# Performance work log

Measured on AMD Instinct MI355X. Metric: run time of the kernel, lower is better.

The kernel has to match this reference:

```python
import jax, jax.numpy as jnp
import numpy as np

B, P, D, K, NCLS = 32, 1024, 3, 5, 2  # graphs, points/graph, input dim, knn, classes
EPS = 1e-5


def _bn(x, g, be):
    # BatchNorm1d in training mode: stats over all axes except channel (torch flattens edges/nodes to rows)
    ax = tuple(range(x.ndim - 1))
    m = jnp.mean(x, axis=ax, keepdims=True)
    v = jnp.mean((x - m) ** 2, axis=ax, keepdims=True)
    return g * (x - m) / jnp.sqrt(v + EPS) + be


def _mlp(x, layers):
    for w, b, g, be in layers:  # Seq(Lin, ReLU, BN)
        x = _bn(jax.nn.relu(x @ w + b), g, be)
    return x


def _knn(x, k):
    # x: [B,P,d] -> idx [B,P,k] of k nearest neighbours (self included, as torch_cluster.knn)
    sq = jnp.sum(x * x, axis=-1)
    d2 = sq[:, :, None] + sq[:, None, :] - 2.0 * jnp.einsum('bpd,bqd->bpq', x, x)
    _, idx = jax.lax.top_k(-d2, k)
    return idx


def _edge_conv(x, k, layers):
    # DynamicEdgeConv: knn graph on current features, msg = nn([x_i, x_j - x_i]), max-aggregate
    idx = _knn(x, k)                                      # [B,P,k]
    xj = jax.vmap(lambda xb, ib: xb[ib])(x, idx)          # [B,P,k,d]
    xi = jnp.broadcast_to(x[:, :, None, :], xj.shape)
    e = jnp.concatenate([xi, xj - xi], axis=-1)           # [B,P,k,2d]
    e = _mlp(e, layers)
    return jnp.max(e, axis=2)                             # max aggr over neighbours


def setup_inputs() -> dict:
    key = jax.random.key(0)
    ks = iter(jax.random.split(key, 40))
    def w(shape):
        return jax.random.normal(next(ks), shape, jnp.float32) * 0.1
    inp = {}
    inp['pos'] = jax.random.normal(next(ks), (B * P, D), jnp.float32)
    inp['batch'] = jnp.repeat(jnp.arange(B, dtype=jnp.int32), P)
    for i, (a, c) in enumerate([(2 * D, 64), (64, 64), (64, 64)], 1):
        inp[f'c1_w{i}'] = w((a, c)); inp[f'c1_b{i}'] = w((c,))
        inp[f'c1_g{i}'] = jnp.ones((c,), jnp.float32); inp[f'c1_be{i}'] = jnp.zeros((c,), jnp.float32)
    inp['c2_w1'] = w((128, 128)); inp['c2_b1'] = w((128,))
    inp['c2_g1'] = jnp.ones((128,), jnp.float32); inp['c2_be1'] = jnp.zeros((128,), jnp.float32)
    inp['l1_w'] = w((192, 1024)); inp['l1_b'] = w((1024,))
    inp['l1_g'] = jnp.ones((1024,), jnp.float32); inp['l1_be'] = jnp.zeros((1024,), jnp.float32)
    inp['m1_w'] = w((1024, 512)); inp['m1_b'] = w((512,))
    inp['m1_g'] = jnp.ones((512,), jnp.float32); inp['m1_be'] = jnp.zeros((512,), jnp.float32)
    inp['m2_w'] = w((512, 256)); inp['m2_b'] = w((256,))
    inp['m2_g'] = jnp.ones((256,), jnp.float32); inp['m2_be'] = jnp.zeros((256,), jnp.float32)
    inp['m3_w'] = w((256, NCLS)); inp['m3_b'] = w((NCLS,))
    return inp


def reference(pos, batch, c1_w1, c1_b1, c1_g1, c1_be1, c1_w2, c1_b2, c1_g2, c1_be2, c1_w3, c1_b3, c1_g3, c1_be3, c2_w1, c2_b1, c2_g1, c2_be1, l1_w, l1_b, l1_g, l1_be, m1_w, m1_b, m1_g, m1_be, m2_w, m2_b, m2_g, m2_be, m3_w, m3_b):
    # equal-sized graphs: batch vector is jnp.repeat(arange(B), P), so reshape is exact
    x = pos.reshape(B, P, D)
    x1 = _edge_conv(x, K, [(c1_w1, c1_b1, c1_g1, c1_be1), (c1_w2, c1_b2, c1_g2, c1_be2), (c1_w3, c1_b3, c1_g3, c1_be3)])  # [B,P,64]
    x2 = _edge_conv(x1, K, [(c2_w1, c2_b1, c2_g1, c2_be1)])  # [B,P,128]
    out = _mlp(jnp.concatenate([x1, x2], axis=-1), [(l1_w, l1_b, l1_g, l1_be)])  # [B,P,1024]
    out = jnp.max(out, axis=1)  # global_max_pool -> [B,1024]
    out = _mlp(out, [(m1_w, m1_b, m1_g, m1_be), (m2_w, m2_b, m2_g, m2_be)])
    return out @ m3_w + m3_b  # [B, n_classes]
```

## Files before the change

kernel.cpp:

```cpp
#include <hip/hip_runtime.h>


#define NB 32
#define NP 1024
#define NPT 32768
#define KNN 5
#define NE 163840

#define FINF 3.402823466e+38f

typedef __attribute__((ext_vector_type(8))) short bf16x8;
typedef __attribute__((ext_vector_type(4))) float f32x4;

__device__ __forceinline__ bool lex_less(float da, int ja, float db, int jb) {
  return (da < db) || (da == db && ja < jb);
}

__device__ __forceinline__ float f4c(const float4& v, int q) {
  return q == 0 ? v.x : (q == 1 ? v.y : (q == 2 ? v.z : v.w));
}

__device__ __forceinline__ ushort f2bf(float f) {
  union { float f; unsigned u; } v; v.f = f;
  unsigned r = (v.u + 0x7FFFu + ((v.u >> 16) & 1u)) >> 16;
  return (ushort)r;
}
__device__ __forceinline__ float bf2f(ushort h) {
  union { unsigned u; float f; } v; v.u = ((unsigned)h) << 16;
  return v.f;
}

__device__ __forceinline__ void insert5(float& d0, float& d1, float& d2, float& d3, float& d4,
                                        int& j0, int& j1, int& j2, int& j3, int& j4,
                                        float dd, int jj) {
  if (lex_less(dd, jj, d4, j4)) {
    bool L0 = lex_less(dd,jj,d0,j0), L1 = lex_less(dd,jj,d1,j1),
         L2 = lex_less(dd,jj,d2,j2), L3 = lex_less(dd,jj,d3,j3);
    d4 = L3 ? d3 : dd;              j4 = L3 ? j3 : jj;
    d3 = L3 ? (L2 ? d2 : dd) : d3;  j3 = L3 ? (L2 ? j2 : jj) : j3;
    d2 = L2 ? (L1 ? d1 : dd) : d2;  j2 = L2 ? (L1 ? j1 : jj) : j2;
    d1 = L1 ? (L0 ? d0 : dd) : d1;  j1 = L1 ? (L0 ? j0 : jj) : j1;
    d0 = L0 ? dd : d0;              j0 = L0 ? jj : j0;
  }
}

__device__ __forceinline__ void insert5f(float& d0, float& d1, float& d2, float& d3, float& d4,
                                         int& j0, int& j1, int& j2, int& j3, int& j4,
                                         float dd, int jj) {
  if (dd < d4) {
    bool L0 = dd < d0, L1 = dd < d1, L2 = dd < d2, L3 = dd < d3;
    d4 = L3 ? d3 : dd;              j4 = L3 ? j3 : jj;
    d3 = L3 ? (L2 ? d2 : dd) : d3;  j3 = L3 ? (L2 ? j2 : jj) : j3;
    d2 = L2 ? (L1 ? d1 : dd) : d2;  j2 = L2 ? (L1 ? j1 : jj) : j2;
    d1 = L1 ? (L0 ? d0 : dd) : d1;  j1 = L1 ? (L0 ? j0 : jj) : j1;
    d0 = L0 ? dd : d0;              j0 = L0 ? jj : j0;
  }
}

__global__ __launch_bounds__(256) void knn1_kernel(const float* __restrict__ pos,
                                                   int* __restrict__ knn_idx) {
  __shared__ float4 xs4[NP];
  const int b = blockIdx.x >> 5;
  const int seg = blockIdx.x & 31;
  const int t = threadIdx.x;
  for (int i = t; i < NP; i += 256) {
    float x0 = pos[(size_t)b*NP*3 + i*3 + 0];
    float x1 = pos[(size_t)b*NP*3 + i*3 + 1];
    float x2 = pos[(size_t)b*NP*3 + i*3 + 2];
    float sq = __fadd_rn(__fadd_rn(__fmul_rn(x0,x0), __fmul_rn(x1,x1)), __fmul_rn(x2,x2));
    xs4[i] = make_float4(x0, x1, x2, sq);
  }
  __syncthreads();
  const int q = t >> 3;
  const int ql = t & 7;
  const int i = seg * 32 + q;
  const float4 xi = xs4[i];
  const float sqi = xi.w;
  float d0=FINF,d1=FINF,d2=FINF,d3=FINF,d4=FINF;
  int j0=0x7fffffff,j1=0x7fffffff,j2=0x7fffffff,j3=0x7fffffff,j4=0x7fffffff;
  for (int jj = 0; jj < NP/8; ++jj) {
    const int j = jj*8 + ql;
    float4 v = xs4[j];
    float dot = __fadd_rn(__fadd_rn(__fmul_rn(xi.x,v.x), __fmul_rn(xi.y,v.y)), __fmul_rn(xi.z,v.z));
    float dd = __fsub_rn(__fadd_rn(sqi, v.w), __fmul_rn(2.0f, dot));
    insert5f(d0,d1,d2,d3,d4, j0,j1,j2,j3,j4, dd, j);
  }
  #pragma unroll
  for (int m = 1; m <= 4; m <<= 1) {
    float e0 = __shfl_xor(d0, m, 8), e1 = __shfl_xor(d1, m, 8),
          e2 = __shfl_xor(d2, m, 8), e3 = __shfl_xor(d3, m, 8),
          e4 = __shfl_xor(d4, m, 8);
    int   k0 = __shfl_xor(j0, m, 8), k1 = __shfl_xor(j1, m, 8),
          k2 = __shfl_xor(j2, m, 8), k3 = __shfl_xor(j3, m, 8),
          k4 = __shfl_xor(j4, m, 8);
    insert5(d0,d1,d2,d3,d4, j0,j1,j2,j3,j4, e0, k0);
    insert5(d0,d1,d2,d3,d4, j0,j1,j2,j3,j4, e1, k1);
    insert5(d0,d1,d2,d3,d4, j0,j1,j2,j3,j4, e2, k2);
    insert5(d0,d1,d2,d3,d4, j0,j1,j2,j3,j4, e3, k3);
    insert5(d0,d1,d2,d3,d4, j0,j1,j2,j3,j4, e4, k4);
  }
  if (ql == 0) {
    const size_t row = (size_t)b * NP + i;
    knn_idx[row*KNN+0] = b*NP + j0;
    knn_idx[row*KNN+1] = b*NP + j1;
    knn_idx[row*KNN+2] = b*NP + j2;
    knn_idx[row*KNN+3] = b*NP + j3;
    knn_idx[row*KNN+4] = b*NP + j4;
  }
}

__global__ __launch_bounds__(256) void ec1_l1_kernel(const float* __restrict__ pos,
    const int* __restrict__ knn_idx, const float* __restrict__ W,
    const float* __restrict__ bias, float* __restrict__ hout,
    double* __restrict__ psum, double* __restrict__ psq) {
  __shared__ float ef[64][6];
  __shared__ float Wl[6][64];
  __shared__ float bl[64];
  __shared__ double red[256];
  const int blk = blockIdx.x, t = threadIdx.x;
  const int ebase = blk * 64;
  if (t < 64) {
    int e = ebase + t;
    int ip = e / KNN;
    int jp = knn_idx[e];
    float a0 = pos[(size_t)ip*3+0], a1 = pos[(size_t)ip*3+1], a2 = pos[(size_t)ip*3+2];
    float c0 = pos[(size_t)jp*3+0], c1 = pos[(size_t)jp*3+1], c2 = pos[(size_t)jp*3+2];
    ef[t][0] = a0; ef[t][1] = a1; ef[t][2] = a2;
    ef[t][3] = c0 - a0; ef[t][4] = c1 - a1; ef[t][5] = c2 - a2;
    bl[t] = bias[t];
  }
  for (int idx = t; idx < 6*64; idx += 256) Wl[idx>>6][idx&63] = W[idx];
  __syncthreads();
  const int c = t & 63, rs = t >> 6;
  double s = 0.0, ss = 0.0;
  for (int r = rs; r < 64; r += 4) {
    float acc = bl[c];
    #pragma unroll
    for (int q = 0; q < 6; ++q) acc = fmaf(ef[r][q], Wl[q][c], acc);
    acc = fmaxf(acc, 0.0f);
    hout[(size_t)(ebase + r)*64 + c] = acc;
    s += acc; ss += (double)acc * (double)acc;
  }
  red[t] = s; __syncthreads();
  if (t < 64) psum[(size_t)blk*64 + t] = red[t] + red[t+64] + red[t+128] + red[t+192];
  __syncthreads();
  red[t] = ss; __syncthreads();
  if (t < 64) psq[(size_t)blk*64 + t] = red[t] + red[t+64] + red[t+128] + red[t+192];
}

__global__ __launch_bounds__(256) void stats_reduce_kernel(const double* __restrict__ psum,
    const double* __restrict__ psq, int nblk, int C, double invN,
    const float* __restrict__ g, const float* __restrict__ be,
    float2* __restrict__ aff) {
  __shared__ double rs[256];
  __shared__ double rq[256];
  const int c = blockIdx.x;
  const int t = threadIdx.x;
  double s = 0.0, ss = 0.0;
  for (int i = t; i < nblk; i += 256) {
    s  += psum[(size_t)i*C + c];
    ss += psq [(size_t)i*C + c];
  }
  rs[t] = s; rq[t] = ss; __syncthreads();
  for (int off = 128; off > 0; off >>= 1) {
    if (t < off) { rs[t] += rs[t+off]; rq[t] += rq[t+off]; }
    __syncthreads();
  }
  if (t == 0) {
    double mean = rs[0] * invN;
    double var = rq[0] * invN - mean*mean;
    var = var < 0.0 ? 0.0 : var;
    double inv = 1.0 / sqrt(var + 1e-5);
    float a = (float)((double)g[c] * inv);
    float off2 = (float)((double)be[c] - (double)g[c] * mean * inv);
    aff[c] = make_float2(a, off2);
  }
}

__global__ __launch_bounds__(256) void ec_l64_kernel(const float* __restrict__ hin,
    const float2* __restrict__ affprev, const float* __restrict__ W,
    const float* __restrict__ bias, float* __restrict__ hout,
    double* __restrict__ psum, double* __restrict__ psq) {
  __shared__ float ein[64][68];
  __shared__ float Wl[64][64];
  __shared__ float2 affl[64];
  __shared__ float bl[64];
  __shared__ double redS[16][64];
  __shared__ double redQ[16][64];
  const int blk = blockIdx.x, t = threadIdx.x;
  const size_t ebase = (size_t)blk * 64;
  if (t < 64) { affl[t] = affprev[t]; bl[t] = bias[t]; }
  __syncthreads();
  for (int idx = t; idx < 64*64; idx += 256) {
    int r = idx >> 6, c = idx & 63;
    float2 ac = affl[c];
    ein[r][c] = fmaf(hin[ebase*64 + idx], ac.x, ac.y);
    Wl[r][c] = W[idx];
  }
  __syncthreads();
  const int c4 = t & 15, rs = t >> 4;
  const int cbase = c4 * 4;
  const int rbase = rs * 4;
  float acc[4][4];
  #pragma unroll
  for (int ii = 0; ii < 4; ++ii) {
    #pragma unroll
    for (int jj = 0; jj < 4; ++jj) acc[ii][jj] = bl[cbase + jj];
  }
  for (int cin = 0; cin < 64; cin += 4) {
    float4 fi[4];
    #pragma unroll
    for (int ii = 0; ii < 4; ++ii) fi[ii] = *(const float4*)&ein[rbase+ii][cin];
    #pragma unroll
    for (int q = 0; q < 4; ++q) {
      float4 wv = *(const float4*)&Wl[cin+q][cbase];
      #pragma unroll
      for (int ii = 0; ii < 4; ++ii) {
        float f = f4c(fi[ii], q);
        acc[ii][0] = fmaf(f, wv.x, acc[ii][0]);
        acc[ii][1] = fmaf(f, wv.y, acc[ii][1]);
        acc[ii][2] = fmaf(f, wv.z, acc[ii][2]);
        acc[ii][3] = fmaf(f, wv.w, acc[ii][3]);
      }
    }
  }
  double s[4] = {0,0,0,0}, ss[4] = {0,0,0,0};
  #pragma unroll
  for (int ii = 0; ii < 4; ++ii) {
    float4 h;
    h.x = fmaxf(acc[ii][0], 0.f); h.y = fmaxf(acc[ii][1], 0.f);
    h.z = fmaxf(acc[ii][2], 0.f); h.w = fmaxf(acc[ii][3], 0.f);
    *(float4*)&hout[(ebase + rbase + ii)*64 + cbase] = h;
    s[0]+=h.x; s[1]+=h.y; s[2]+=h.z; s[3]+=h.w;
    ss[0]+=(double)h.x*h.x; ss[1]+=(double)h.y*h.y;
    ss[2]+=(double)h.z*h.z; ss[3]+=(double)h.w*h.w;
  }
  #pragma unroll
  for (int jj = 0; jj < 4; ++jj) { redS[rs][cbase+jj] = s[jj]; redQ[rs][cbase+jj] = ss[jj]; }
  __syncthreads();
  if (t < 64) {
    double a = 0, bq = 0;
    #pragma unroll
    for (int r = 0; r < 16; ++r) { a += redS[r][t]; bq += redQ[r][t]; }
    psum[(size_t)blk*64 + t] = a;
    psq[(size_t)blk*64 + t] = bq;
  }
}

__global__ __launch_bounds__(256) void ec_l64_last_kernel(const float* __restrict__ hin,
    const float2* __restrict__ affprev, const float* __restrict__ W,
    const float* __restrict__ bias, float* __restrict__ hmax, float* __restrict__ hmin,
    double* __restrict__ psum, double* __restrict__ psq) {
  __shared__ float ein[80][68];
  __shared__ float Wl[64][64];
  __shared__ float2 affl[64];
  __shared__ float bl[64];
  double (*redS)[64] = (double (*)[64])(&ein[0][0]);
  double (*redQ)[64] = (double (*)[64])((char*)&ein[0][0] + 8192);
  const int blk = blockIdx.x, t = threadIdx.x;
  const size_t ebase = (size_t)blk * 80;
  if (t < 64) { affl[t] = affprev[t]; bl[t] = bias[t]; }
  __syncthreads();
  for (int idx = t; idx < 80*64; idx += 256) {
    int r = idx >> 6, c = idx & 63;
    float2 ac = affl[c];
    ein[r][c] = fmaf(hin[ebase*64 + idx], ac.x, ac.y);
  }
  for (int idx = t; idx < 64*64; idx += 256) Wl[idx>>6][idx&63] = W[idx];
  __syncthreads();
  const int c4 = t & 15, rs = t >> 4;
  const int cbase = c4 * 4;
  const int rbase = rs * 5;
  float acc[5][4];
  #pragma unroll
  for (int ii = 0; ii < 5; ++ii) {
    #pragma unroll
    for (int jj = 0; jj < 4; ++jj) acc[ii][jj] = bl[cbase + jj];
  }
  for (int cin = 0; cin < 64; cin += 4) {
    float4 fi[5];
    #pragma unroll
    for (int ii = 0; ii < 5; ++ii) fi[ii] = *(const float4*)&ein[rbase+ii][cin];
    #pragma unroll
    for (int q = 0; q < 4; ++q) {
      float4 wv = *(const float4*)&Wl[cin+q][cbase];
      #pragma unroll
      for (int ii = 0; ii < 5; ++ii) {
        float f = f4c(fi[ii], q);
        acc[ii][0] = fmaf(f, wv.x, acc[ii][0]);
        acc[ii][1] = fmaf(f, wv.y, acc[ii][1]);
        acc[ii][2] = fmaf(f, wv.z, acc[ii][2]);
        acc[ii][3] = fmaf(f, wv.w, acc[ii][3]);
      }
    }
  }
  float4 mx = make_float4(-FINF,-FINF,-FINF,-FINF);
  float4 mn = make_float4(FINF,FINF,FINF,FINF);
  double s[4] = {0,0,0,0}, ss[4] = {0,0,0,0};
  #pragma unroll
  for (int ii = 0; ii < 5; ++ii) {
    float4 h;
    h.x = fmaxf(acc[ii][0], 0.f); h.y = fmaxf(acc[ii][1], 0.f);
    h.z = fmaxf(acc[ii][2], 0.f); h.w = fmaxf(acc[ii][3], 0.f);
    mx.x = fmaxf(mx.x, h.x); mn.x = fminf(mn.x, h.x);
    mx.y = fmaxf(mx.y, h.y); mn.y = fminf(mn.y, h.y);
    mx.z = fmaxf(mx.z, h.z); mn.z = fminf(mn.z, h.z);
    mx.w = fmaxf(mx.w, h.w); mn.w = fminf(mn.w, h.w);
    s[0]+=h.x; s[1]+=h.y; s[2]+=h.z; s[3]+=h.w;
    ss[0]+=(double)h.x*h.x; ss[1]+=(double)h.y*h.y;
    ss[2]+=(double)h.z*h.z; ss[3]+=(double)h.w*h.w;
  }
  *(float4*)&hmax[((size_t)blk*16 + rs)*64 + cbase] = mx;
  *(float4*)&hmin[((size_t)blk*16 + rs)*64 + cbase] = mn;
  __syncthreads();
  #pragma unroll
  for (int jj = 0; jj < 4; ++jj) { redS[rs][cbase+jj] = s[jj]; redQ[rs][cbase+jj] = ss[jj]; }
  __syncthreads();
  if (t < 64) {
    double a = 0, bq = 0;
    #pragma unroll
    for (int r = 0; r < 16; ++r) { a += redS[r][t]; bq += redQ[r][t]; }
    psum[(size_t)blk*64 + t] = a;
    psq[(size_t)blk*64 + t] = bq;
  }
}

__global__ __launch_bounds__(256) void x1c_kernel(const float* __restrict__ hmax,
    const float* __restrict__ hmin, const float2* __restrict__ aff,
    float* __restrict__ x1, ushort* __restrict__ x1hi, ushort* __restrict__ x1lo,
    float* __restrict__ sqg) {
  __shared__ float xs[16][65];
  const int blk = blockIdx.x, t = threadIdx.x;
  const size_t base = (size_t)blk * 16 * 64;
  const int o = t * 4;
  const int c4 = o & 63;
  float4 vmx = *(const float4*)&hmax[base + o];
  float4 vmn = *(const float4*)&hmin[base + o];
  float2 a0 = aff[c4+0], a1 = aff[c4+1], a2 = aff[c4+2], a3 = aff[c4+3];
  float4 xv;
  xv.x = (a0.x >= 0.f) ? fmaf(a0.x, vmx.x, a0.y) : fmaf(a0.x, vmn.x, a0.y);
  xv.y = (a1.x >= 0.f) ? fmaf(a1.x, vmx.y, a1.y) : fmaf(a1.x, vmn.y, a1.y);
  xv.z = (a2.x >= 0.f) ? fmaf(a2.x, vmx.z, a2.y) : fmaf(a2.x, vmn.z, a2.y);
  xv.w = (a3.x >= 0.f) ? fmaf(a3.x, vmx.w, a3.y) : fmaf(a3.x, vmn.w, a3.y);
  *(float4*)&x1[base + o] = xv;
  ushort4 h, lo;
  h.x = f2bf(xv.x); lo.x = f2bf(xv.x - bf2f(h.x));
  h.y = f2bf(xv.y); lo.y = f2bf(xv.y - bf2f(h.y));
  h.z = f2bf(xv.z); lo.z = f2bf(xv.z - bf2f(h.z));
  h.w = f2bf(xv.w); lo.w = f2bf(xv.w - bf2f(h.w));
  *(ushort4*)&x1hi[base + o] = h;
  *(ushort4*)&x1lo[base + o] = lo;
  const int r = o >> 6;
  xs[r][c4+0] = xv.x; xs[r][c4+1] = xv.y; xs[r][c4+2] = xv.z; xs[r][c4+3] = xv.w;
  __syncthreads();
  if (t < 16) {
    float s = 0.f;
    #pragma unroll
    for (int c = 0; c < 64; ++c) s = fmaf(xs[t][c], xs[t][c], s);
    sqg[(size_t)blk*16 + t] = s;
  }
}

__global__ __launch_bounds__(256) void knn2_kernel(const ushort* __restrict__ x1hi,
    const ushort* __restrict__ x1lo, const float* __restrict__ sqg,
    float* __restrict__ kpd, int* __restrict__ kpj) {
  __shared__ __align__(16) char smem[36864];
  ushort* xihi = (ushort*)smem;
  ushort* xilo = (ushort*)(smem + 9216);
  ushort* xjhi = (ushort*)(smem + 18432);
  ushort* xjlo = (ushort*)(smem + 27648);
  float*  dist = (float*)(smem + 18432);
  const int b = blockIdx.x >> 5;
  const int it = (blockIdx.x >> 1) & 15;
  const int half = blockIdx.x & 1;
  const int t = threadIdx.x;
  const int ibase = it * 64;

  #pragma unroll
  for (int i = 0; i < 2; ++i) {
    int idx = i*256 + t;
    int r = idx >> 3, c8 = (idx & 7) * 8;
    *(bf16x8*)&xihi[r*72 + c8] = *(const bf16x8*)&x1hi[((size_t)b*NP + ibase + r)*64 + c8];
    *(bf16x8*)&xilo[r*72 + c8] = *(const bf16x8*)&x1lo[((size_t)b*NP + ibase + r)*64 + c8];
  }

  const int w = t >> 6, l = t & 63;
  const int lr = l & 15, lg = l >> 4;
  const int row = t >> 2, ql = t & 3;
  float si2[4];
  #pragma unroll
  for (int ii = 0; ii < 4; ++ii)
    si2[ii] = sqg[(size_t)b*NP + ibase + w*16 + lg*4 + ii];

  float d0=FINF,d1=FINF,d2=FINF,d3=FINF,d4=FINF;
  int j0=0x7fffffff,j1=0x7fffffff,j2=0x7fffffff,j3=0x7fffffff,j4=0x7fffffff;

  for (int jt = 0; jt < 8; ++jt) {
    const int jtg = half * 8 + jt;
    __syncthreads();
    #pragma unroll
    for (int i = 0; i < 2; ++i) {
      int idx = i*256 + t;
      int r = idx >> 3, c8 = (idx & 7) * 8;
      *(bf16x8*)&xjhi[r*72 + c8] = *(const bf16x8*)&x1hi[((size_t)b*NP + jtg*64 + r)*64 + c8];
      *(bf16x8*)&xjlo[r*72 + c8] = *(const bf16x8*)&x1lo[((size_t)b*NP + jtg*64 + r)*64 + c8];
    }
    __syncthreads();
    f32x4 acc0 = (f32x4){0.f,0.f,0.f,0.f};
    f32x4 acc1 = (f32x4){0.f,0.f,0.f,0.f};
    f32x4 acc2 = (f32x4){0.f,0.f,0.f,0.f};
    f32x4 acc3 = (f32x4){0.f,0.f,0.f,0.f};
    #pragma unroll
    for (int ks = 0; ks < 2; ++ks) {
      const int k0 = ks * 32;
      bf16x8 ah = *(const bf16x8*)&xihi[(w*16 + lr)*72 + k0 + lg*8];
      bf16x8 al = *(const bf16x8*)&xilo[(w*16 + lr)*72 + k0 + lg*8];
      {
        bf16x8 bh = *(const bf16x8*)&xjhi[(0*16 + lr)*72 + k0 + lg*8];
        bf16x8 bl = *(const bf16x8*)&xjlo[(0*16 + lr)*72 + k0 + lg*8];
        acc0 = __builtin_amdgcn_mfma_f32_16x16x32_bf16(ah, bh, acc0, 0, 0, 0);
        acc0 = __builtin_amdgcn_mfma_f32_16x16x32_bf16(ah, bl, acc0, 0, 0, 0);
        acc0 = __builtin_amdgcn_mfma_f32_16x16x32_bf16(al, bh, acc0, 0, 0, 0);
        acc0 = __builtin_amdgcn_mfma_f32_16x16x32_bf16(al, bl, acc0, 0, 0, 0);
      }
      {
        bf16x8 bh = *(const bf16x8*)&xjhi[(1*16 + lr)*72 + k0 + lg*8];
        bf16x8 bl = *(const bf16x8*)&xjlo[(1*16 + lr)*72 + k0 + lg*8];
        acc1 = __builtin_amdgcn_mfma_f32_16x16x32_bf16(ah, bh, acc1, 0, 0, 0);
        acc1 = __builtin_amdgcn_mfma_f32_16x16x32_bf16(ah, bl, acc1, 0, 0, 0);
        acc1 = __builtin_amdgcn_mfma_f32_16x16x32_bf16(al, bh, acc1, 0, 0, 0);
        acc1 = __builtin_amdgcn_mfma_f32_16x16x32_bf16(al, bl, acc1, 0, 0, 0);
      }
      {
        bf16x8 bh = *(const bf16x8*)&xjhi[(2*16 + lr)*72 + k0 + lg*8];
        bf16x8 bl = *(const bf16x8*)&xjlo[(2*16 + lr)*72 + k0 + lg*8];
        acc2 = __builtin_amdgcn_mfma_f32_16x16x32_bf16(ah, bh, acc2, 0, 0, 0);
        acc2 = __builtin_amdgcn_mfma_f32_16x16x32_bf16(ah, bl, acc2, 0, 0, 0);
        acc2 = __builtin_amdgcn_mfma_f32_16x16x32_bf16(al, bh, acc2, 0, 0, 0);
        acc2 = __builtin_amdgcn_mfma_f32_16x16x32_bf16(al, bl, acc2, 0, 0, 0);
      }
      {
        bf16x8 bh = *(const bf16x8*)&xjhi[(3*16 + lr)*72 + k0 + lg*8];
        bf16x8 bl = *(const bf16x8*)&xjlo[(3*16 + lr)*72 + k0 + lg*8];
        acc3 = __builtin_amdgcn_mfma_f32_16x16x32_bf16(ah, bh, acc3, 0, 0, 0);
        acc3 = __builtin_amdgcn_mfma_f32_16x16x32_bf16(ah, bl, acc3, 0, 0, 0);
        acc3 = __builtin_amdgcn_mfma_f32_16x16x32_bf16(al, bh, acc3, 0, 0, 0);
        acc3 = __builtin_amdgcn_mfma_f32_16x16x32_bf16(al, bl, acc3, 0, 0, 0);
      }
    }
    float sjv0 = sqg[(size_t)b*NP + jtg*64 + 0*16 + lr];
    float sjv1 = sqg[(size_t)b*NP + jtg*64 + 1*16 + lr];
    float sjv2 = sqg[(size_t)b*NP + jtg*64 + 2*16 + lr];
    float sjv3 = sqg[(size_t)b*NP + jtg*64 + 3*16 + lr];
    __syncthreads();
    #pragma unroll
    for (int ii = 0; ii < 4; ++ii) {
      const int irow = w*16 + lg*4 + ii;
      dist[irow*68 + 0*16 + lr] = fmaf(-2.f, acc0[ii], si2[ii] + sjv0);
      dist[irow*68 + 1*16 + lr] = fmaf(-2.f, acc1[ii], si2[ii] + sjv1);
      dist[irow*68 + 2*16 + lr] = fmaf(-2.f, acc2[ii], si2[ii] + sjv2);
      dist[irow*68 + 3*16 + lr] = fmaf(-2.f, acc3[ii], si2[ii] + sjv3);
    }
    __syncthreads();
    const int jgbase = jtg*64 + ql*16;
    #pragma unroll
    for (int kk = 0; kk < 4; ++kk) {
      float4 v = *(const float4*)&dist[row*68 + ql*16 + 4*kk];
      insert5f(d0,d1,d2,d3,d4, j0,j1,j2,j3,j4, v.x, jgbase + 4*kk + 0);
      insert5f(d0,d1,d2,d3,d4, j0,j1,j2,j3,j4, v.y, jgbase + 4*kk + 1);
      insert5f(d0,d1,d2,d3,d4, j0,j1,j2,j3,j4, v.z, jgbase + 4*kk + 2);
      insert5f(d0,d1,d2,d3,d4, j0,j1,j2,j3,j4, v.w, jgbase + 4*kk + 3);
    }
  }

  #pragma unroll
  for (int m = 1; m <= 2; m <<= 1) {
    float e0 = __shfl_xor(d0, m, 4), e1 = __shfl_xor(d1, m, 4),
          e2 = __shfl_xor(d2, m, 4), e3 = __shfl_xor(d3, m, 4),
          e4 = __shfl_xor(d4, m, 4);
    int   k0 = __shfl_xor(j0, m, 4), k1 = __shfl_xor(j1, m, 4),
          k2 = __shfl_xor(j2, m, 4), k3 = __shfl_xor(j3, m, 4),
          k4 = __shfl_xor(j4, m, 4);
    insert5(d0,d1,d2,d3,d4, j0,j1,j2,j3,j4, e0, k0);
    insert5(d0,d1,d2,d3,d4, j0,j1,j2,j3,j4, e1, k1);
    insert5(d0,d1,d2,d3,d4, j0,j1,j2,j3,j4, e2, k2);
    insert5(d0,d1,d2,d3,d4, j0,j1,j2,j3,j4, e3, k3);
    insert5(d0,d1,d2,d3,d4, j0,j1,j2,j3,j4, e4, k4);
  }
  if (ql == 0) {
    const size_t orow = ((size_t)half*NPT + (size_t)b*NP + ibase + row) * KNN;
    kpd[orow+0] = d0; kpd[orow+1] = d1; kpd[orow+2] = d2; kpd[orow+3] = d3; kpd[orow+4] = d4;
    kpj[orow+0] = j0; kpj[orow+1] = j1; kpj[orow+2] = j2; kpj[orow+3] = j3; kpj[orow+4] = j4;
  }
}

__global__ void knn2_merge_kernel(const float* __restrict__ kpd,
    const int* __restrict__ kpj, int* __restrict__ knn_idx) {
  int r = blockIdx.x * 256 + threadIdx.x;
  if (r >= NPT) return;
  const int b = r >> 10;
  const size_t r0 = (size_t)r * KNN;
  const size_t r1 = ((size_t)NPT + r) * KNN;
  float d0 = kpd[r0+0], d1 = kpd[r0+1], d2 = kpd[r0+2], d3 = kpd[r0+3], d4 = kpd[r0+4];
  int   j0 = kpj[r0+0], j1 = kpj[r0+1], j2 = kpj[r0+2], j3 = kpj[r0+3], j4 = kpj[r0+4];
  #pragma unroll
  for (int s = 0; s < KNN; ++s) {
    insert5(d0,d1,d2,d3,d4, j0,j1,j2,j3,j4, kpd[r1+s], kpj[r1+s]);
  }
  knn_idx[r0+0] = b*NP + j0;
  knn_idx[r0+1] = b*NP + j1;
  knn_idx[r0+2] = b*NP + j2;
  knn_idx[r0+3] = b*NP + j3;
  knn_idx[r0+4] = b*NP + j4;
}

__global__ __launch_bounds__(256) void wt2_kernel(const float* __restrict__ W,
    ushort* __restrict__ WthiF, ushort* __restrict__ WtloF) {
  __shared__ ushort lsh[64][128];
  __shared__ ushort lsl[64][128];
  const int cbase = blockIdx.x * 64;
  const int t = threadIdx.x;
  for (int idx = t; idx < 128 * 64; idx += 256) {
    int cc = idx & 63, k = idx >> 6;
    float w = W[(size_t)k * 128 + cbase + cc];
    ushort hi = f2bf(w);
    ushort lo = f2bf(w - bf2f(hi));
    lsh[cc][k] = hi; lsl[cc][k] = lo;
  }
  __syncthreads();
  const int ctl = t >> 6, lane = t & 63;
  const int lr = lane & 15, lg = lane >> 4;
  const int ctg = (cbase >> 4) + ctl;
  #pragma unroll
  for (int ks = 0; ks < 4; ++ks) {
    size_t o = ((size_t)(ctg*4 + ks)*64 + lane) * 8;
    *(bf16x8*)&WthiF[o] = *(const bf16x8*)&lsh[ctl*16 + lr][ks*32 + lg*8];
    *(bf16x8*)&WtloF[o] = *(const bf16x8*)&lsl[ctl*16 + lr][ks*32 + lg*8];
  }
}

#define EC2S 136
__global__ __launch_bounds__(256) void ec2_kernel(const float* __restrict__ x1,
    const int* __restrict__ knn_idx, const ushort* __restrict__ WthiF,
    const ushort* __restrict__ WtloF, const float* __restrict__ bias,
    float* __restrict__ x2max, float* __restrict__ x2min,
    double* __restrict__ psum, double* __restrict__ psq) {
  __shared__ __align__(16) char smem[2 * 40 * EC2S * 2];
  ushort* Ahi = (ushort*)smem;
  ushort* Alo = (ushort*)(smem + 40 * EC2S * 2);
  float (*outs)[132] = (float (*)[132])smem;
  double (*redS)[128] = (double (*)[128])smem;
  double (*redQ)[128] = (double (*)[128])(smem + 4*128*8);
  const int blk = blockIdx.x, t = threadIdx.x;
  const int pbase = blk * 8;
  for (int idx = t; idx < 40 * 32; idx += 256) {
    int r = idx >> 5, c4 = (idx & 31) * 4;
    int p = pbase + r / KNN;
    int kk = r % KNN;
    float4 v;
    if (c4 < 64) {
      v = *(const float4*)&x1[(size_t)p * 64 + c4];
    } else {
      int cc = c4 - 64;
      int j = knn_idx[(size_t)p * KNN + kk];
      float4 vj = *(const float4*)&x1[(size_t)j * 64 + cc];
      float4 vp = *(const float4*)&x1[(size_t)p * 64 + cc];
      v = make_float4(vj.x - vp.x, vj.y - vp.y, vj.z - vp.z, vj.w - vp.w);
    }
    ushort4 h, lo;
    h.x = f2bf(v.x); lo.x = f2bf(v.x - bf2f(h.x));
    h.y = f2bf(v.y); lo.y = f2bf(v.y - bf2f(h.y));
    h.z = f2bf(v.z); lo.z = f2bf(v.z - bf2f(h.z));
    h.w = f2bf(v.w); lo.w = f2bf(v.w - bf2f(h.w));
    *(ushort4*)&Ahi[r * EC2S + c4] = h;
    *(ushort4*)&Alo[r * EC2S + c4] = lo;
  }
  __syncthreads();
  const int l = t & 63, w = t >> 6;
  const int lr = l & 15, lg = l >> 4;
  f32x4 acc[3][2];
  #pragma unroll
  for (int rt = 0; rt < 3; ++rt) {
    acc[rt][0] = (f32x4){0.f,0.f,0.f,0.f};
    acc[rt][1] = (f32x4){0.f,0.f,0.f,0.f};
  }
  #pragma unroll
  for (int ks = 0; ks < 4; ++ks) {
    const int k0 = ks * 32;
    bf16x8 bh0 = *(const bf16x8*)&WthiF[((size_t)((2*w  )*4 + ks)*64 + l)*8];
    bf16x8 bh1 = *(const bf16x8*)&WthiF[((size_t)((2*w+1)*4 + ks)*64 + l)*8];
    bf16x8 bl0 = *(const bf16x8*)&WtloF[((size_t)((2*w  )*4 + ks)*64 + l)*8];
    bf16x8 bl1 = *(const bf16x8*)&WtloF[((size_t)((2*w+1)*4 + ks)*64 + l)*8];
    #pragma unroll
    for (int rt = 0; rt < 3; ++rt) {
      int ar = rt*16 + lr;
      int arc = ar < 40 ? ar : 39;
      bf16x8 ah = *(const bf16x8*)&Ahi[arc * EC2S + k0 + lg*8];
      bf16x8 al = *(const bf16x8*)&Alo[arc * EC2S + k0 + lg*8];
      acc[rt][0] = __builtin_amdgcn_mfma_f32_16x16x32_bf16(ah, bh0, acc[rt][0], 0, 0, 0);
      acc[rt][0] = __builtin_amdgcn_mfma_f32_16x16x32_bf16(ah, bl0, acc[rt][0], 0, 0, 0);
      acc[rt][0] = __builtin_amdgcn_mfma_f32_16x16x32_bf16(al, bh0, acc[rt][0], 0, 0, 0);
      acc[rt][1] = __builtin_amdgcn_mfma_f32_16x16x32_bf16(ah, bh1, acc[rt][1], 0, 0, 0);
      acc[rt][1] = __builtin_amdgcn_mfma_f32_16x16x32_bf16(ah, bl1, acc[rt][1], 0, 0, 0);
      acc[rt][1] = __builtin_amdgcn_mfma_f32_16x16x32_bf16(al, bh1, acc[rt][1], 0, 0, 0);
    }
  }
  __syncthreads();
  {
    const float bv0 = bias[w*32 + lr];
    const float bv1 = bias[w*32 + 16 + lr];
    #pragma unroll
    for (int rt = 0; rt < 3; ++rt) {
      #pragma unroll
      for (int i = 0; i < 4; ++i) {
        int e = rt*16 + lg*4 + i;
        if (e < 40) {
          outs[e][w*32 + lr]      = fmaxf(acc[rt][0][i] + bv0, 0.f);
          outs[e][w*32 + 16 + lr] = fmaxf(acc[rt][1][i] + bv1, 0.f);
        }
      }
    }
  }
  __syncthreads();
  double s4[4] = {0,0,0,0}, q4[4] = {0,0,0,0};
  {
    const int p = t >> 5;
    const int cs = (t & 31) * 4;
    float4 mx = make_float4(-FINF,-FINF,-FINF,-FINF);
    float4 mn = make_float4(FINF,FINF,FINF,FINF);
    #pragma unroll
    for (int kk = 0; kk < KNN; ++kk) {
      float4 va = *(const float4*)&outs[p*KNN + kk][cs];
      mx.x = fmaxf(mx.x, va.x); mn.x = fminf(mn.x, va.x); s4[0] += va.x; q4[0] += (double)va.x*va.x;
      mx.y = fmaxf(mx.y, va.y); mn.y = fminf(mn.y, va.y); s4[1] += va.y; q4[1] += (double)va.y*va.y;
      mx.z = fmaxf(mx.z, va.z); mn.z = fminf(mn.z, va.z); s4[2] += va.z; q4[2] += (double)va.z*va.z;
      mx.w = fmaxf(mx.w, va.w); mn.w = fminf(mn.w, va.w); s4[3] += va.w; q4[3] += (double)va.w*va.w;
    }
    *(float4*)&x2max[((size_t)pbase + p)*128 + cs] = mx;
    *(float4*)&x2min[((size_t)pbase + p)*128 + cs] = mn;
    #pragma unroll
    for (int cc = 0; cc < 4; ++cc) {
      s4[cc] += __shfl_xor(s4[cc], 32);
      q4[cc] += __shfl_xor(q4[cc], 32);
    }
  }
  __syncthreads();
  {
    const int cs = (t & 31) * 4;
    if ((t & 63) < 32) {
      #pragma unroll
      for (int cc = 0; cc < 4; ++cc) {
        redS[t >> 6][cs + cc] = s4[cc];
        redQ[t >> 6][cs + cc] = q4[cc];
      }
    }
  }
  __syncthreads();
  if (t < 128) {
    double a = redS[0][t] + redS[1][t] + redS[2][t] + redS[3][t];
    double q = redQ[0][t] + redQ[1][t] + redQ[2][t] + redQ[3][t];
    psum[(size_t)blk*128 + t] = a;
    psq [(size_t)blk*128 + t] = q;
  }
}

__global__ void x2c_kernel(const float* __restrict__ x2max,
    const float* __restrict__ x2min, const float2* __restrict__ aff2,
    ushort* __restrict__ x2bf) {
  int idx = blockIdx.x * 256 + threadIdx.x;
  int o = idx * 4;
  int c4 = o & 127;
  float4 vmx = *(const float4*)&x2max[o];
  float4 vmn = *(const float4*)&x2min[o];
  float2 a0 = aff2[c4+0], a1 = aff2[c4+1], a2 = aff2[c4+2], a3 = aff2[c4+3];
  ushort4 hv;
  hv.x = f2bf((a0.x >= 0.f) ? fmaf(a0.x, vmx.x, a0.y) : fmaf(a0.x, vmn.x, a0.y));
  hv.y = f2bf((a1.x >= 0.f) ? fmaf(a1.x, vmx.y, a1.y) : fmaf(a1.x, vmn.y, a1.y));
  hv.z = f2bf((a2.x >= 0.f) ? fmaf(a2.x, vmx.z, a2.y) : fmaf(a2.x, vmn.z, a2.y));
  hv.w = f2bf((a3.x >= 0.f) ? fmaf(a3.x, vmx.w, a3.y) : fmaf(a3.x, vmn.w, a3.y));
  *(ushort4*)&x2bf[o] = hv;
}

__global__ __launch_bounds__(256) void wt_kernel(const float* __restrict__ W,
                                                 ushort* __restrict__ WtF) {
  __shared__ ushort ls[64][192];
  const int cbase = blockIdx.x * 64;
  const int t = threadIdx.x;
  for (int idx = t; idx < 192 * 64; idx += 256) {
    int cc = idx & 63, k = idx >> 6;
    ls[cc][k] = f2bf(W[(size_t)k * 1024 + cbase + cc]);
  }
  __syncthreads();
  const int ctl = t >> 6, lane = t & 63;
  const int lr = lane & 15, lg = lane >> 4;
  const int ctg = (cbase >> 4) + ctl;
  #pragma unroll
  for (int ks = 0; ks < 6; ++ks) {
    size_t o = ((size_t)(ctg*6 + ks)*64 + lane) * 8;
    *(bf16x8*)&WtF[o] = *(const bf16x8*)&ls[ctl*16 + lr][ks*32 + lg*8];
  }
}

__global__ __launch_bounds__(256) void lin1_kernel(const ushort* __restrict__ x1hi,
    const ushort* __restrict__ x2bf, const ushort* __restrict__ WtF,
    const float* __restrict__ bias, double* __restrict__ psum,
    double* __restrict__ psq, float* __restrict__ pmax, float* __restrict__ pmin) {
  __shared__ ushort As[64 * 208];
  const int blk = blockIdx.x, t = threadIdx.x;
  const int brow = blk >> 1;
  const int ch = blk & 1;
  const int pbase = brow * 64;
  #pragma unroll
  for (int i = 0; i < 2; ++i) {
    int idx = i*256 + t;
    int r = idx >> 3, c8 = (idx & 7) * 8;
    *(bf16x8*)&As[r*208 + c8] = *(const bf16x8*)&x1hi[((size_t)pbase + r)*64 + c8];
  }
  #pragma unroll
  for (int i = 0; i < 4; ++i) {
    int idx = i*256 + t;
    int r = idx >> 4, c8 = (idx & 15) * 8;
    *(bf16x8*)&As[r*208 + 64 + c8] = *(const bf16x8*)&x2bf[((size_t)pbase + r)*128 + c8];
  }
  __syncthreads();
  const int l = t & 63, w = t >> 6;
  const int lr = l & 15, lg = l >> 4;
  f32x4 acc[8][4];
  #pragma unroll
  for (int ct = 0; ct < 8; ++ct) {
    #pragma unroll
    for (int rf = 0; rf < 4; ++rf) acc[ct][rf] = (f32x4){0.f, 0.f, 0.f, 0.f};
  }
  #pragma unroll
  for (int ks = 0; ks < 6; ++ks) {
    const int k0 = ks * 32;
    bf16x8 a0 = *(const bf16x8*)&As[( 0 + lr) * 208 + k0 + lg * 8];
    bf16x8 a1 = *(const bf16x8*)&As[(16 + lr) * 208 + k0 + lg * 8];
    bf16x8 a2 = *(const bf16x8*)&As[(32 + lr) * 208 + k0 + lg * 8];
    bf16x8 a3 = *(const bf16x8*)&As[(48 + lr) * 208 + k0 + lg * 8];
    #pragma unroll
    for (int ct = 0; ct < 8; ++ct) {
      bf16x8 bv = *(const bf16x8*)&WtF[((size_t)((ch*32 + w*8 + ct)*6 + ks)*64 + l)*8];
      acc[ct][0] = __builtin_amdgcn_mfma_f32_16x16x32_bf16(a0, bv, acc[ct][0], 0, 0, 0);
      acc[ct][1] = __builtin_amdgcn_mfma_f32_16x16x32_bf16(a1, bv, acc[ct][1], 0, 0, 0);
      acc[ct][2] = __builtin_amdgcn_mfma_f32_16x16x32_bf16(a2, bv, acc[ct][2], 0, 0, 0);
      acc[ct][3] = __builtin_amdgcn_mfma_f32_16x16x32_bf16(a3, bv, acc[ct][3], 0, 0, 0);
    }
  }
  #pragma unroll
  for (int ct = 0; ct < 8; ++ct) {
    const int c = ch*512 + w*128 + ct * 16 + lr;
    const float bv = bias[c];
    double s = 0.0, ss = 0.0;
    float mx = -FINF, mn = FINF;
    #pragma unroll
    for (int rf = 0; rf < 4; ++rf) {
      #pragma unroll
      for (int i = 0; i < 4; ++i) {
        float h = fmaxf(acc[ct][rf][i] + bv, 0.f);
        s += (double)h;
        ss += (double)h * h;
        mx = fmaxf(mx, h);
        mn = fminf(mn, h);
      }
    }
    s  += __shfl_xor(s, 16);  ss += __shfl_xor(ss, 16);
    mx = fmaxf(mx, __shfl_xor(mx, 16)); mn = fminf(mn, __shfl_xor(mn, 16));
    s  += __shfl_xor(s, 32);  ss += __shfl_xor(ss, 32);
    mx = fmaxf(mx, __shfl_xor(mx, 32)); mn = fminf(mn, __shfl_xor(mn, 32));
    if (lg == 0) {
      psum[(size_t)brow * 1024 + c] = s;
      psq [(size_t)brow * 1024 + c] = ss;
      pmax[(size_t)brow * 1024 + c] = mx;
      pmin[(size_t)brow * 1024 + c] = mn;
    }
  }
}

__global__ __launch_bounds__(256) void lin1_fin_kernel(const double* __restrict__ psum,
    const double* __restrict__ psq, const float* __restrict__ pmax,
    const float* __restrict__ pmin, const float* __restrict__ g,
    const float* __restrict__ be, float* __restrict__ y) {
  __shared__ double rs[256];
  __shared__ double rq[256];
  __shared__ float smx[32][8];
  __shared__ float smn[32][8];
  __shared__ float sa[2];
  const int c = blockIdx.x;
  const int t = threadIdx.x;
  double s = 0.0, ss = 0.0;
  for (int i = t; i < 512; i += 256) {
    s  += psum[(size_t)i*1024 + c];
    ss += psq [(size_t)i*1024 + c];
  }
  rs[t] = s; rq[t] = ss; __syncthreads();
  for (int off = 128; off > 0; off >>= 1) {
    if (t < off) { rs[t] += rs[t+off]; rq[t] += rq[t+off]; }
    __syncthreads();
  }
  if (t == 0) {
    double mean = rs[0] / 32768.0;
    double var = rq[0] / 32768.0 - mean*mean;
    var = var < 0.0 ? 0.0 : var;
    double inv = 1.0 / sqrt(var + 1e-5);
    sa[0] = (float)((double)g[c] * inv);
    sa[1] = (float)((double)be[c] - (double)g[c]*mean*inv);
  }
  {
    int b = t >> 3, q = t & 7;
    float mxv = -FINF, mnv = FINF;
    #pragma unroll
    for (int k = 0; k < 2; ++k) {
      int i = b*16 + q*2 + k;
      mxv = fmaxf(mxv, pmax[(size_t)i*1024 + c]);
      mnv = fminf(mnv, pmin[(size_t)i*1024 + c]);
    }
    smx[b][q] = mxv;
    smn[b][q] = mnv;
  }
  __syncthreads();
  if (t < 32) {
    float mxv = -FINF, mnv = FINF;
    #pragma unroll
    for (int q = 0; q < 8; ++q) { mxv = fmaxf(mxv, smx[t][q]); mnv = fminf(mnv, smn[t][q]); }
    float a = sa[0], off2 = sa[1];
    y[(size_t)t*1024 + c] = (a >= 0.f) ? fmaf(a, mxv, off2) : fmaf(a, mnv, off2);
  }
}

__global__ __launch_bounds__(256) void head1_kernel(const float* __restrict__ y,
    const float* __restrict__ W, const float* __restrict__ bias, float* __restrict__ h5) {
  __shared__ float yr[1024];
  __shared__ float part[256];
  const int r = blockIdx.x >> 2;
  const int cseg = (blockIdx.x & 3) * 128;
  const int t = threadIdx.x;
  for (int i = t; i < 1024; i += 256) yr[i] = y[(size_t)r*1024 + i];
  __syncthreads();
  const int c = cseg + (t & 127);
  const int kh = t >> 7;
  const int kbase = kh * 512;
  float a0 = 0.f, a1 = 0.f, a2 = 0.f, a3 = 0.f;
  for (int cin = 0; cin < 512; cin += 4) {
    a0 = fmaf(yr[kbase+cin+0], W[(size_t)(kbase+cin+0)*512 + c], a0);
    a1 = fmaf(yr[kbase+cin+1], W[(size_t)(kbase+cin+1)*512 + c], a1);
    a2 = fmaf(yr[kbase+cin+2], W[(size_t)(kbase+cin+2)*512 + c], a2);
    a3 = fmaf(yr[kbase+cin+3], W[(size_t)(kbase+cin+3)*512 + c], a3);
  }
  part[t] = ((a0 + a1) + (a2 + a3));
  __syncthreads();
  if (t < 128) {
    float acc = bias[c] + part[t] + part[t + 128];
    h5[(size_t)r*512 + c] = fmaxf(acc, 0.f);
  }
}

__global__ void bn_rows_kernel(const float* __restrict__ h, int C, int R,
    const float* __restrict__ g, const float* __restrict__ be, float2* __restrict__ aff) {
  int c = blockIdx.x*256 + threadIdx.x;
  if (c >= C) return;
  double s = 0, ss = 0;
  for (int r = 0; r < R; ++r) {
    double v = (double)h[(size_t)r*C + c];
    s += v; ss += v*v;
  }
  double mean = s / (double)R;
  double var = ss / (double)R - mean*mean;
  var = var < 0.0 ? 0.0 : var;
  double inv = 1.0 / sqrt(var + 1e-5);
  float a = (float)((double)g[c] * inv);
  float off = (float)((double)be[c] - (double)g[c]*mean*inv);
  aff[c] = make_float2(a, off);
}

__global__ __launch_bounds__(256) void head2_kernel(const float* __restrict__ h5,
    const float2* __restrict__ aff, const float* __restrict__ W,
    const float* __restrict__ bias, float* __restrict__ h6) {
  __shared__ float hr[512];
  const int r = blockIdx.x;
  const int t = threadIdx.x;
  for (int i = t; i < 512; i += 256) {
    float2 a = aff[i];
    hr[i] = fmaf(a.x, h5[(size_t)r*512 + i], a.y);
  }
  __syncthreads();
  const int c = t;
  float a0 = 0.f, a1 = 0.f, a2 = 0.f, a3 = 0.f;
  for (int cin = 0; cin < 512; cin += 4) {
    a0 = fmaf(hr[cin+0], W[(size_t)(cin+0)*256 + c], a0);
    a1 = fmaf(hr[cin+1], W[(size_t)(cin+1)*256 + c], a1);
    a2 = fmaf(hr[cin+2], W[(size_t)(cin+2)*256 + c], a2);
    a3 = fmaf(hr[cin+3], W[(size_t)(cin+3)*256 + c], a3);
  }
  float acc = bias[c] + ((a0 + a1) + (a2 + a3));
  h6[(size_t)r*256 + c] = fmaxf(acc, 0.f);
}

__global__ void head3_kernel(const float* __restrict__ h6, const float2* __restrict__ aff,
    const float* __restrict__ W, const float* __restrict__ bias, float* __restrict__ out) {
  int t = threadIdx.x;
  if (t >= 64) return;
  int r = t >> 1, c = t & 1;
  float acc = bias[c];
  for (int cin = 0; cin < 256; ++cin) {
    float2 a = aff[cin];
    acc = fmaf(fmaf(a.x, h6[(size_t)r*256 + cin], a.y), W[(size_t)cin*2 + c], acc);
  }
  out[(size_t)r*2 + c] = acc;
}

extern "C" void kernel_launch(void* const* d_in, const int* in_sizes, int n_in,
                              void* d_out, int out_size, void* d_ws, size_t ws_size,
                              hipStream_t stream) {
  (void)in_sizes; (void)n_in; (void)out_size; (void)ws_size;
  const float* pos    = (const float*)d_in[0];
  const float* c1_w1  = (const float*)d_in[2];
  const float* c1_b1  = (const float*)d_in[3];
  const float* c1_g1  = (const float*)d_in[4];
  const float* c1_be1 = (const float*)d_in[5];
  const float* c1_w2  = (const float*)d_in[6];
  const float* c1_b2  = (const float*)d_in[7];
  const float* c1_g2  = (const float*)d_in[8];
  const float* c1_be2 = (const float*)d_in[9];
  const float* c1_w3  = (const float*)d_in[10];
  const float* c1_b3  = (const float*)d_in[11];
  const float* c1_g3  = (const float*)d_in[12];
  const float* c1_be3 = (const float*)d_in[13];
  const float* c2_w1  = (const float*)d_in[14];
  const float* c2_b1  = (const float*)d_in[15];
  const float* c2_g1  = (const float*)d_in[16];
  const float* c2_be1 = (const float*)d_in[17];
  const float* l1_w   = (const float*)d_in[18];
  const float* l1_b   = (const float*)d_in[19];
  const float* l1_g   = (const float*)d_in[20];
  const float* l1_be  = (const float*)d_in[21];
  const float* m1_w   = (const float*)d_in[22];
  const float* m1_b   = (const float*)d_in[23];
  const float* m1_g   = (const float*)d_in[24];
  const float* m1_be  = (const float*)d_in[25];
  const float* m2_w   = (const float*)d_in[26];
  const float* m2_b   = (const float*)d_in[27];
  const float* m2_g   = (const float*)d_in[28];
  const float* m2_be  = (const float*)d_in[29];
  const float* m3_w   = (const float*)d_in[30];
  const float* m3_b   = (const float*)d_in[31];

  char* ws = (char*)d_ws;
  size_t off = 0;
  auto alloc = [&](size_t bytes) -> void* {
    void* p = ws + off;
    off += (bytes + 255) & ~(size_t)255;
    return p;
  };
  int*    idx1 = (int*)alloc((size_t)NE * 4);
  int*    idx2 = (int*)alloc((size_t)NE * 4);
  float*  x1   = (float*)alloc((size_t)NPT * 64 * 4);
  float*  hA   = (float*)alloc((size_t)NE * 64 * 4);
  float*  hB   = (float*)alloc((size_t)NE * 64 * 4);
  double* psum = (double*)alloc((size_t)1048576 * 8);
  double* psq  = (double*)alloc((size_t)1048576 * 8);
  float*  pmax = (float*)alloc((size_t)1048576 * 4);
  float*  pmin = (float*)alloc((size_t)1048576 * 4);
  float2* affA = (float2*)alloc(64 * 8);
  float2* affB = (float2*)alloc(64 * 8);
  float2* affC = (float2*)alloc(64 * 8);
  float2* aff2 = (float2*)alloc(128 * 8);
  float2* affM1 = (float2*)alloc(512 * 8);
  float2* affM2 = (float2*)alloc(256 * 8);
  float*  y    = (float*)alloc((size_t)NB * 1024 * 4);
  float*  h5   = (float*)alloc((size_t)NB * 512 * 4);
  float*  h6   = (float*)alloc((size_t)NB * 256 * 4);
  ushort* WtF  = (ushort*)alloc((size_t)1024 * 192 * 2);
  ushort* Wt2hiF = (ushort*)alloc((size_t)128 * 128 * 2);
  ushort* Wt2loF = (ushort*)alloc((size_t)128 * 128 * 2);
  float*  sqg  = (float*)alloc((size_t)NPT * 4);
  ushort* x1hi = (ushort*)alloc((size_t)NPT * 64 * 2);
  ushort* x1lo = (ushort*)alloc((size_t)NPT * 64 * 2);
  ushort* x2bf = (ushort*)alloc((size_t)NPT * 128 * 2);
  float*  kpd  = (float*)alloc((size_t)2 * NPT * KNN * 4);
  int*    kpj  = (int*)alloc((size_t)2 * NPT * KNN * 4);
  float* hmax = hA;
  float* hmin = hA + (size_t)NPT * 64;
  float* x2max = hA;
  float* x2min = hA + (size_t)NPT * 128;

  wt_kernel<<<dim3(16), dim3(256), 0, stream>>>(l1_w, WtF);
  wt2_kernel<<<dim3(2), dim3(256), 0, stream>>>(c2_w1, Wt2hiF, Wt2loF);
  knn1_kernel<<<dim3(NB*32), dim3(256), 0, stream>>>(pos, idx1);
  ec1_l1_kernel<<<dim3(NE/64), dim3(256), 0, stream>>>(pos, idx1, c1_w1, c1_b1, hA, psum, psq);
  stats_reduce_kernel<<<dim3(64), dim3(256), 0, stream>>>(psum, psq, NE/64, 64, 1.0/NE, c1_g1, c1_be1, affA);
  ec_l64_kernel<<<dim3(NE/64), dim3(256), 0, stream>>>(hA, affA, c1_w2, c1_b2, hB, psum, psq);
  stats_reduce_kernel<<<dim3(64), dim3(256), 0, stream>>>(psum, psq, NE/64, 64, 1.0/NE, c1_g2, c1_be2, affB);
  ec_l64_last_kernel<<<dim3(NPT/16), dim3(256), 0, stream>>>(hB, affB, c1_w3, c1_b3, hmax, hmin, psum, psq);
  stats_reduce_kernel<<<dim3(64), dim3(256), 0, stream>>>(psum, psq, NPT/16, 64, 1.0/NE, c1_g3, c1_be3, affC);
  x1c_kernel<<<dim3(NPT/16), dim3(256), 0, stream>>>(hmax, hmin, affC, x1, x1hi, x1lo, sqg);
  knn2_kernel<<<dim3(NB*32), dim3(256), 0, stream>>>(x1hi, x1lo, sqg, kpd, kpj);
  knn2_merge_kernel<<<dim3(NPT/256), dim3(256), 0, stream>>>(kpd, kpj, idx2);
  ec2_kernel<<<dim3(NPT/8), dim3(256), 0, stream>>>(x1, idx2, Wt2hiF, Wt2loF, c2_b1, x2max, x2min, psum, psq);
  stats_reduce_kernel<<<dim3(128), dim3(256), 0, stream>>>(psum, psq, NPT/8, 128, 1.0/NE, c2_g1, c2_be1, aff2);
  x2c_kernel<<<dim3(NPT*128/1024), dim3(256), 0, stream>>>(x2max, x2min, aff2, x2bf);
  lin1_kernel<<<dim3(1024), dim3(256), 0, stream>>>(x1hi, x2bf, WtF, l1_b, psum, psq, pmax, pmin);
  lin1_fin_kernel<<<dim3(1024), dim3(256), 0, stream>>>(psum, psq, pmax, pmin, l1_g, l1_be, y);
  head1_kernel<<<dim3(128), dim3(256), 0, stream>>>(y, m1_w, m1_b, h5);
  bn_rows_kernel<<<dim3(2), dim3(256), 0, stream>>>(h5, 512, NB, m1_g, m1_be, affM1);
  head2_kernel<<<dim3(32), dim3(256), 0, stream>>>(h5, affM1, m2_w, m2_b, h6);
  bn_rows_kernel<<<dim3(1), dim3(256), 0, stream>>>(h6, 256, NB, m2_g, m2_be, affM2);
  head3_kernel<<<dim3(1), dim3(64), 0, stream>>>(h6, affM2, m3_w, m3_b, (float*)d_out);
}
```

Measured before the change: 371.0 us.

## Select kNN candidates directly from MFMA accumulators instead of via LDS staging

The knn2 kernel no longer writes the distance tile to shared memory and re-reads it per row. Each lane now keeps four top-5 lists, one per accumulator row, inserting distances straight from the MFMA outputs. The lists are merged with a 16-lane shuffle butterfly at the end. This removes two barriers and the LDS round trip per tile, but raises register use (20 distances plus 20 indices) and adds more shuffle-merge work, which may reduce occupancy.

New measurement: 1.100 ms. +196.5%, slower.

```diff
diff --git a/kernel.cpp b/kernel.cpp
--- a/kernel.cpp
+++ b/kernel.cpp
@@ -369,7 +369,6 @@
   ushort* xilo = (ushort*)(smem + 9216);
   ushort* xjhi = (ushort*)(smem + 18432);
   ushort* xjlo = (ushort*)(smem + 27648);
-  float*  dist = (float*)(smem + 18432);
   const int b = blockIdx.x >> 5;
   const int it = (blockIdx.x >> 1) & 15;
   const int half = blockIdx.x & 1;
@@ -386,14 +385,14 @@
 
   const int w = t >> 6, l = t & 63;
   const int lr = l & 15, lg = l >> 4;
-  const int row = t >> 2, ql = t & 3;
   float si2[4];
   #pragma unroll
   for (int ii = 0; ii < 4; ++ii)
     si2[ii] = sqg[(size_t)b*NP + ibase + w*16 + lg*4 + ii];
 
-  float d0=FINF,d1=FINF,d2=FINF,d3=FINF,d4=FINF;
-  int j0=0x7fffffff,j1=0x7fffffff,j2=0x7fffffff,j3=0x7fffffff,j4=0x7fffffff;
+  float D[20]; int J[20];
+  #pragma unroll
+  for (int k = 0; k < 20; ++k) { D[k] = FINF; J[k] = 0x7fffffff; }
 
   for (int jt = 0; jt < 8; ++jt) {
     const int jtg = half * 8 + jt;
@@ -452,45 +451,55 @@
     float sjv1 = sqg[(size_t)b*NP + jtg*64 + 1*16 + lr];
     float sjv2 = sqg[(size_t)b*NP + jtg*64 + 2*16 + lr];
     float sjv3 = sqg[(size_t)b*NP + jtg*64 + 3*16 + lr];
-    __syncthreads();
+    const int jb = jtg*64 + lr;
     #pragma unroll
     for (int ii = 0; ii < 4; ++ii) {
-      const int irow = w*16 + lg*4 + ii;
-      dist[irow*68 + 0*16 + lr] = fmaf(-2.f, acc0[ii], si2[ii] + sjv0);
-      dist[irow*68 + 1*16 + lr] = fmaf(-2.f, acc1[ii], si2[ii] + sjv1);
-      dist[irow*68 + 2*16 + lr] = fmaf(-2.f, acc2[ii], si2[ii] + sjv2);
-      dist[irow*68 + 3*16 + lr] = fmaf(-2.f, acc3[ii], si2[ii] + sjv3);
-    }
-    __syncthreads();
-    const int jgbase = jtg*64 + ql*16;
-    #pragma unroll
-    for (int kk = 0; kk < 4; ++kk) {
-      float4 v = *(const float4*)&dist[row*68 + ql*16 + 4*kk];
-      insert5f(d0,d1,d2,d3,d4, j0,j1,j2,j3,j4, v.x, jgbase + 4*kk + 0);
-      insert5f(d0,d1,d2,d3,d4, j0,j1,j2,j3,j4, v.y, jgbase + 4*kk + 1);
-      insert5f(d0,d1,d2,d3,d4, j0,j1,j2,j3,j4, v.z, jgbase + 4*kk + 2);
-      insert5f(d0,d1,d2,d3,d4, j0,j1,j2,j3,j4, v.w, jgbase + 4*kk + 3);
-    }
-  }
-
-  #pragma unroll
-  for (int m = 1; m <= 2; m <<= 1) {
-    float e0 = __shfl_xor(d0, m, 4), e1 = __shfl_xor(d1, m, 4),
-          e2 = __shfl_xor(d2, m, 4), e3 = __shfl_xor(d3, m, 4),
-          e4 = __shfl_xor(d4, m, 4);
-    int   k0 = __shfl_xor(j0, m, 4), k1 = __shfl_xor(j1, m, 4),
-          k2 = __shfl_xor(j2, m, 4), k3 = __shfl_xor(j3, m, 4),
-          k4 = __shfl_xor(j4, m, 4);
-    insert5(d0,d1,d2,d3,d4, j0,j1,j2,j3,j4, e0, k0);
-    insert5(d0,d1,d2,d3,d4, j0,j1,j2,j3,j4, e1, k1);
-    insert5(d0,d1,d2,d3,d4, j0,j1,j2,j3,j4, e2, k2);
-    insert5(d0,d1,d2,d3,d4, j0,j1,j2,j3,j4, e3, k3);
-    insert5(d0,d1,d2,d3,d4, j0,j1,j2,j3,j4, e4, k4);
-  }
-  if (ql == 0) {
-    const size_t orow = ((size_t)half*NPT + (size_t)b*NP + ibase + row) * KNN;
-    kpd[orow+0] = d0; kpd[orow+1] = d1; kpd[orow+2] = d2; kpd[orow+3] = d3; kpd[orow+4] = d4;
-    kpj[orow+0] = j0; kpj[orow+1] = j1; kpj[orow+2] = j2; kpj[orow+3] = j3; kpj[orow+4] = j4;
+      float dd0 = fmaf(-2.f, acc0[ii], si2[ii] + sjv0);
+      insert5f(D[ii*5+0],D[ii*5+1],D[ii*5+2],D[ii*5+3],D[ii*5+4],
+               J[ii*5+0],J[ii*5+1],J[ii*5+2],J[ii*5+3],J[ii*5+4], dd0, jb + 0);
+      float dd1 = fmaf(-2.f, acc1[ii], si2[ii] + sjv1);
+      insert5f(D[ii*5+0],D[ii*5+1],D[ii*5+2],D[ii*5+3],D[ii*5+4],
+               J[ii*5+0],J[ii*5+1],J[ii*5+2],J[ii*5+3],J[ii*5+4], dd1, jb + 16);
+      float dd2 = fmaf(-2.f, acc2[ii], si2[ii] + sjv2);
+      insert5f(D[ii*5+0],D[ii*5+1],D[ii*5+2],D[ii*5+3],D[ii*5+4],
+               J[ii*5+0],J[ii*5+1],J[ii*5+2],J[ii*5+3],J[ii*5+4], dd2, jb + 32);
+      float dd3 = fmaf(-2.f, acc3[ii], si2[ii] + sjv3);
+      insert5f(D[ii*5+0],D[ii*5+1],D[ii*5+2],D[ii*5+3],D[ii*5+4],
+               J[ii*5+0],J[ii*5+1],J[ii*5+2],J[ii*5+3],J[ii*5+4], dd3, jb + 48);
+    }
+  }
+
+  #pragma unroll
+  for (int m = 1; m <= 8; m <<= 1) {
+    #pragma unroll
+    for (int ii = 0; ii < 4; ++ii) {
+      float e0 = __shfl_xor(D[ii*5+0], m, 16), e1 = __shfl_xor(D[ii*5+1], m, 16),
+            e2 = __shfl_xor(D[ii*5+2], m, 16), e3 = __shfl_xor(D[ii*5+3], m, 16),
+            e4 = __shfl_xor(D[ii*5+4], m, 16);
+      int   k0 = __shfl_xor(J[ii*5+0], m, 16), k1 = __shfl_xor(J[ii*5+1], m, 16),
+            k2 = __shfl_xor(J[ii*5+2], m, 16), k3 = __shfl_xor(J[ii*5+3], m, 16),
+            k4 = __shfl_xor(J[ii*5+4], m, 16);
+      insert5(D[ii*5+0],D[ii*5+1],D[ii*5+2],D[ii*5+3],D[ii*5+4],
+              J[ii*5+0],J[ii*5+1],J[ii*5+2],J[ii*5+3],J[ii*5+4], e0, k0);
+      insert5(D[ii*5+0],D[ii*5+1],D[ii*5+2],D[ii*5+3],D[ii*5+4],
+              J[ii*5+0],J[ii*5+1],J[ii*5+2],J[ii*5+3],J[ii*5+4], e1, k1);
+      insert5(D[ii*5+0],D[ii*5+1],D[ii*5+2],D[ii*5+3],D[ii*5+4],
+              J[ii*5+0],J[ii*5+1],J[ii*5+2],J[ii*5+3],J[ii*5+4], e2, k2);
+      insert5(D[ii*5+0],D[ii*5+1],D[ii*5+2],D[ii*5+3],D[ii*5+4],
+              J[ii*5+0],J[ii*5+1],J[ii*5+2],J[ii*5+3],J[ii*5+4], e3, k3);
+      insert5(D[ii*5+0],D[ii*5+1],D[ii*5+2],D[ii*5+3],D[ii*5+4],
+              J[ii*5+0],J[ii*5+1],J[ii*5+2],J[ii*5+3],J[ii*5+4], e4, k4);
+    }
+  }
+  if (lr == 0) {
+    #pragma unroll
+    for (int ii = 0; ii < 4; ++ii) {
+      const size_t orow = ((size_t)half*NPT + (size_t)b*NP + ibase + w*16 + lg*4 + ii) * KNN;
+      kpd[orow+0] = D[ii*5+0]; kpd[orow+1] = D[ii*5+1]; kpd[orow+2] = D[ii*5+2];
+      kpd[orow+3] = D[ii*5+3]; kpd[orow+4] = D[ii*5+4];
+      kpj[orow+0] = J[ii*5+0]; kpj[orow+1] = J[ii*5+1]; kpj[orow+2] = J[ii*5+2];
+      kpj[orow+3] = J[ii*5+3]; kpj[orow+4] = J[ii*5+4];
+    }
   }
 }
 
```
